# Performance work log

Hardware: AMD Instinct MI355X
Metric: run time of the kernel (lower is better)

The kernel has to match this reference:

```python
import jax, jax.numpy as jnp
import numpy as np

B, X, Y, Z, CIN = 4, 64, 64, 64, 32
COUT = 32
MX, MY, MZ = 16, 16, 16


def setup_inputs() -> dict:
    key = jax.random.key(0)
    k1, k2, k3 = jax.random.split(key, 3)
    x = jax.random.normal(k1, (B, X, Y, Z, CIN), dtype=jnp.float32)
    # Glorot-uniform-like scale for (in, out, mx, my, mz) weights
    fan = CIN + COUT
    lim = np.sqrt(6.0 / fan).astype(np.float32)
    w_real = jax.random.uniform(k2, (CIN, COUT, MX, MY, MZ), minval=-lim, maxval=lim, dtype=jnp.float32)
    w_imag = jax.random.uniform(k3, (CIN, COUT, MX, MY, MZ), minval=-lim, maxval=lim, dtype=jnp.float32)
    return {"x": x, "w_real": w_real, "w_imag": w_imag}


def reference(x, w_real, w_imag):
    # tf.signal.fft3d transforms the innermost 3 axes of the 5D input:
    # x is [B, X, Y, Z, C] so the FFT runs over (Y, Z, C) -- faithful to source.
    x_ft = jnp.fft.fftn(x.astype(jnp.complex64), axes=(-3, -2, -1))
    x_ft = jnp.transpose(x_ft, (0, 4, 1, 2, 3))            # [B, C, X, Y, Z]
    mx, my, mz = w_real.shape[2], w_real.shape[3], w_real.shape[4]
    x_crop = x_ft[:, :, :mx, :my, :mz]                     # [B, Cin, mx, my, mz]
    w = jax.lax.complex(w_real, w_imag)                    # [Cin, Cout, mx, my, mz]
    out_ft = jnp.einsum('bixyz,ioxyz->boxyz', x_crop, w)   # [B, Cout, mx, my, mz]
    sx, sy, sz = x.shape[1], x.shape[2], x.shape[3]
    out_ft = jnp.pad(out_ft, ((0, 0), (0, 0), (0, sx - mx), (0, sy - my), (0, sz - mz)))
    out_ft = jnp.transpose(out_ft, (0, 2, 3, 4, 1))        # [B, X, Y, Z, Cout]
    x_out = jnp.fft.ifftn(out_ft, axes=(-3, -2, -1))
    return jnp.real(x_out)
```

## Files before the change

kernel.cpp:

```cpp
#include <hip/hip_runtime.h>
#include <math.h>

#define PI_F 3.14159265358979323846f


__global__ __launch_bounds__(256) void k_dft_z(const float* __restrict__ x,
                                               float2* __restrict__ T1) {
    int bid = blockIdx.x;
    int ih = bid & 1, yg = (bid >> 1) & 7, xx = (bid >> 4) & 15, b = bid >> 8;
    __shared__ float  sx[8192];
    __shared__ float2 twt[1024];
    float4* sx4 = (float4*)sx;
    const float4* src4 = (const float4*)(x + (size_t)((b * 64 + xx) * 64 + yg * 8) * 2048) + ih * 4;
    #pragma unroll
    for (int t = threadIdx.x; t < 2048; t += 256) {
        int i4 = t & 3, z = (t >> 2) & 63, y = t >> 8;
        sx4[(y * 64 + z) * 4 + i4] = src4[(size_t)y * 512 + z * 8 + i4];
    }
    const float cn = -2.0f * PI_F / 64.0f;
    for (int t = threadIdx.x; t < 1024; t += 256) {
        int z = t >> 4, kz = t & 15;
        float a = cn * (float)((z * kz) & 63);
        twt[t] = make_float2(__cosf(a), __sinf(a));
    }
    __syncthreads();
    int ig = threadIdx.x & 3, kz2 = (threadIdx.x >> 2) & 7, y8 = threadIdx.x >> 5;
    float ar0[4], ai0[4], ar1[4], ai1[4];
    #pragma unroll
    for (int j = 0; j < 4; j++) { ar0[j] = ai0[j] = ar1[j] = ai1[j] = 0.f; }
    const float4* twv = (const float4*)twt;
    #pragma unroll 8
    for (int z = 0; z < 64; z++) {
        float4 va = sx4[(y8 * 64 + z) * 4 + ig];
        float4 tp = twv[z * 8 + kz2];
        float v[4] = {va.x, va.y, va.z, va.w};
        #pragma unroll
        for (int j = 0; j < 4; j++) {
            ar0[j] = fmaf(v[j], tp.x, ar0[j]);
            ai0[j] = fmaf(v[j], tp.y, ai0[j]);
            ar1[j] = fmaf(v[j], tp.z, ar1[j]);
            ai1[j] = fmaf(v[j], tp.w, ai1[j]);
        }
    }
    int y = yg * 8 + y8, kz0 = kz2 * 2, i0 = ih * 16 + ig * 4;
    float2* dst = T1 + (size_t)((b * 16 + xx) * 64 + y) * 512;
    float4* d0 = (float4*)(dst + kz0 * 32 + i0);
    d0[0] = make_float4(ar0[0], ai0[0], ar0[1], ai0[1]);
    d0[1] = make_float4(ar0[2], ai0[2], ar0[3], ai0[3]);
    float4* d1 = (float4*)(dst + (kz0 + 1) * 32 + i0);
    d1[0] = make_float4(ar1[0], ai1[0], ar1[1], ai1[1]);
    d1[1] = make_float4(ar1[2], ai1[2], ar1[3], ai1[3]);
}

__global__ __launch_bounds__(256) void k_dft_y(const float2* __restrict__ T1,
                                               float2* __restrict__ XH) {
    int bid = blockIdx.x;
    int ih = bid & 1, kzg = (bid >> 1) & 3, xx = (bid >> 3) & 15, b = bid >> 7;
    __shared__ float4 sT4[2304];
    __shared__ float2 twt[1024];
    const float4* Tg4 = (const float4*)T1;
    size_t gbase = (size_t)(b * 16 + xx) * 64 * 256;
    #pragma unroll
    for (int t = threadIdx.x; t < 2048; t += 256) {
        int i4 = t & 7, kz4 = (t >> 3) & 3, y = t >> 5;
        sT4[kz4 * 576 + y * 9 + i4] =
            Tg4[gbase + (size_t)y * 256 + (kzg * 4 + kz4) * 16 + ih * 8 + i4];
    }
    const float cn = -2.0f * PI_F / 64.0f;
    for (int t = threadIdx.x; t < 1024; t += 256) {
        int y = t >> 4, ky = t & 15;
        float a = cn * (float)((y * ky) & 63);
        twt[t] = make_float2(__cosf(a), __sinf(a));
    }
    __syncthreads();
    int ig = threadIdx.x & 7, ky2 = (threadIdx.x >> 3) & 7, kz4 = threadIdx.x >> 6;
    float ar[2][2], ai[2][2];
    #pragma unroll
    for (int h = 0; h < 2; h++) { ar[h][0] = ar[h][1] = ai[h][0] = ai[h][1] = 0.f; }
    const float4* twv = (const float4*)twt;
    #pragma unroll 8
    for (int y = 0; y < 64; y++) {
        float4 a  = sT4[kz4 * 576 + y * 9 + ig];
        float4 tp = twv[y * 8 + ky2];
        float xr[2] = {a.x, a.z}, xi[2] = {a.y, a.w};
        #pragma unroll
        for (int j = 0; j < 2; j++) {
            ar[0][j] += xr[j] * tp.x - xi[j] * tp.y;
            ai[0][j] += xr[j] * tp.y + xi[j] * tp.x;
            ar[1][j] += xr[j] * tp.z - xi[j] * tp.w;
            ai[1][j] += xr[j] * tp.w + xi[j] * tp.z;
        }
    }
    int kz = kzg * 4 + kz4;
    #pragma unroll
    for (int h = 0; h < 2; h++) {
        int ky = ky2 * 2 + h;
        float2* dp = XH + (((size_t)(b * 16 + xx) * 16 + ky) * 16 + kz) * 32 + ih * 16 + ig * 2;
        *(float4*)dp = make_float4(ar[h][0], ai[h][0], ar[h][1], ai[h][1]);
    }
}

__global__ __launch_bounds__(512) void k_mid(const float2* __restrict__ XH,
                                             const float* __restrict__ wr,
                                             const float* __restrict__ wi,
                                             float2* __restrict__ G,
                                             float* __restrict__ out) {
    int bid = blockIdx.x;
    if (bid >= 256) {
        int f = bid - 256;
        int b = f / 384, rem = f - b * 384;
        float4* d4 = (float4*)(out + (size_t)(b * 64 + 16) * 131072) + (size_t)rem * 4096;
        #pragma unroll
        for (int r = 0; r < 8; ++r)
            d4[r * 512 + threadIdx.x] = make_float4(0.f, 0.f, 0.f, 0.f);
        return;
    }
    int ky = bid & 15, xx = bid >> 4;
    __shared__ float2 sA[4 * 528];
    __shared__ float2 sB[4 * 576];
    __shared__ float2 twt[1024];
    for (int t = threadIdx.x; t < 2048; t += 512) {
        int b = t >> 9, kz = (t >> 5) & 15, i = t & 31;
        sA[b * 528 + kz * 33 + i] =
            XH[(((size_t)(b * 16 + xx) * 16 + ky) * 16 + kz) * 32 + i];
    }
    const float cn32 = -2.0f * PI_F / 32.0f;
    for (int t = threadIdx.x; t < 1024; t += 512) {
        int m = t >> 5, k = t & 31;
        float a = cn32 * (float)((m * k) & 31);
        twt[t] = make_float2(__cosf(a), __sinf(a));
    }
    __syncthreads();
    const float4* twv = (const float4*)twt;
    {
        int kz = threadIdx.x & 15, kig = (threadIdx.x >> 4) & 7, b = threadIdx.x >> 7;
        float xr[4], xi[4];
        #pragma unroll
        for (int j = 0; j < 4; j++) { xr[j] = xi[j] = 0.f; }
        #pragma unroll 8
        for (int i = 0; i < 32; i++) {
            float2 a   = sA[b * 528 + kz * 33 + i];
            float4 tp0 = twv[i * 16 + kig * 2];
            float4 tp1 = twv[i * 16 + kig * 2 + 1];
            xr[0] += a.x * tp0.x - a.y * tp0.y;  xi[0] += a.x * tp0.y + a.y * tp0.x;
            xr[1] += a.x * tp0.z - a.y * tp0.w;  xi[1] += a.x * tp0.w + a.y * tp0.z;
            xr[2] += a.x * tp1.x - a.y * tp1.y;  xi[2] += a.x * tp1.y + a.y * tp1.x;
            xr[3] += a.x * tp1.z - a.y * tp1.w;  xi[3] += a.x * tp1.w + a.y * tp1.z;
        }
        #pragma unroll
        for (int j = 0; j < 4; j++)
            sB[b * 576 + (kig * 4 + j) * 18 + kz] = make_float2(xr[j], xi[j]);
    }
    __syncthreads();
    {
        int kzg = threadIdx.x & 3, o = (threadIdx.x >> 2) & 31, b = threadIdx.x >> 7;
        int wbase = xx * 256 + ky * 16 + kzg * 4;
        float Fr[4], Fi[4];
        #pragma unroll
        for (int q = 0; q < 4; q++) { Fr[q] = Fi[q] = 0.f; }
        const float4* sB4 = (const float4*)sB;
        #pragma unroll 4
        for (int ki = 0; ki < 32; ki++) {
            float4 a01 = sB4[b * 288 + ki * 9 + kzg * 2];
            float4 a23 = sB4[b * 288 + ki * 9 + kzg * 2 + 1];
            float4 w4r = *(const float4*)(wr + (size_t)(ki * 32 + o) * 4096 + wbase);
            float4 w4i = *(const float4*)(wi + (size_t)(ki * 32 + o) * 4096 + wbase);
            float xr[4]  = {a01.x, a01.z, a23.x, a23.z};
            float xi[4]  = {a01.y, a01.w, a23.y, a23.w};
            float wrv[4] = {w4r.x, w4r.y, w4r.z, w4r.w};
            float wiv[4] = {w4i.x, w4i.y, w4i.z, w4i.w};
            #pragma unroll
            for (int q = 0; q < 4; q++) {
                Fr[q] += xr[q] * wrv[q] - xi[q] * wiv[q];
                Fi[q] += xr[q] * wiv[q] + xi[q] * wrv[q];
            }
        }
        #pragma unroll
        for (int q = 0; q < 4; q++) {
            int kz = kzg * 4 + q;
            sA[b * 528 + kz * 33 + o] = make_float2(Fr[q], Fi[q]);
        }
    }
    __syncthreads();
    {
        int kz = threadIdx.x & 15, cog = (threadIdx.x >> 4) & 7, b = threadIdx.x >> 7;
        float gr[4], gi[4];
        #pragma unroll
        for (int j = 0; j < 4; j++) { gr[j] = gi[j] = 0.f; }
        #pragma unroll 8
        for (int o = 0; o < 32; o++) {
            float2 f   = sA[b * 528 + kz * 33 + o];
            float4 tp0 = twv[o * 16 + cog * 2];
            float4 tp1 = twv[o * 16 + cog * 2 + 1];
            gr[0] += f.x * tp0.x + f.y * tp0.y;  gi[0] += f.y * tp0.x - f.x * tp0.y;
            gr[1] += f.x * tp0.z + f.y * tp0.w;  gi[1] += f.y * tp0.z - f.x * tp0.w;
            gr[2] += f.x * tp1.x + f.y * tp1.y;  gi[2] += f.y * tp1.x - f.x * tp1.y;
            gr[3] += f.x * tp1.z + f.y * tp1.w;  gi[3] += f.y * tp1.z - f.x * tp1.w;
        }
        float2* dp = G + (((size_t)(b * 16 + xx) * 16 + ky) * 16 + kz) * 32 + cog * 4;
        ((float4*)dp)[0] = make_float4(gr[0], gi[0], gr[1], gi[1]);
        ((float4*)dp)[1] = make_float4(gr[2], gi[2], gr[3], gi[3]);
    }
}

__global__ __launch_bounds__(256) void k_idft_zy(const float2* __restrict__ G,
                                                 float* __restrict__ out) {
    int bid = blockIdx.x;
    int ch = bid & 1, zc = (bid >> 1) & 7, xx = (bid >> 4) & 15, b = bid >> 8;
    float* dstb = out + (size_t)(b * 64 + xx) * 131072;
    __shared__ float2 sH[128 * 17];
    __shared__ float2 twy[1024];
    __shared__ float2 twz[8 * 17];
    const float cp = 2.0f * PI_F / 64.0f;
    for (int t = threadIdx.x; t < 1024; t += 256) {
        int ky = t >> 6, y = t & 63;
        float a = cp * (float)((ky * y) & 63);
        twy[t] = make_float2(__cosf(a), __sinf(a));
    }
    if (threadIdx.x < 128) {
        int dz = threadIdx.x >> 4, kz = threadIdx.x & 15;
        int z = zc * 8 + dz;
        float a = cp * (float)((kz * z) & 63);
        twz[dz * 17 + kz] = make_float2(__cosf(a), __sinf(a));
    }
    __syncthreads();
    {
        int co = threadIdx.x & 15, dz = (threadIdx.x >> 4) & 7, kyg = threadIdx.x >> 7;
        float tzc[16], tzs[16];
        #pragma unroll
        for (int kz = 0; kz < 16; ++kz) {
            float2 t = twz[dz * 17 + kz];
            tzc[kz] = t.x; tzs[kz] = t.y;
        }
        const float2* Gb0 = G + (size_t)(b * 16 + xx) * 16 * 512 + ch * 16 + co;
        #pragma unroll
        for (int t = 0; t < 8; ++t) {
            int ky = kyg * 8 + t;
            const float2* Gk = Gb0 + (size_t)ky * 512;
            float hr = 0.f, hi = 0.f;
            #pragma unroll
            for (int kz = 0; kz < 16; ++kz) {
                float2 g = Gk[kz * 32];
                hr += g.x * tzc[kz] - g.y * tzs[kz];
                hi += g.x * tzs[kz] + g.y * tzc[kz];
            }
            sH[(ky * 8 + dz) * 17 + co] = make_float2(hr, hi);
        }
    }
    __syncthreads();
    {
        int cog = threadIdx.x & 1, dz = (threadIdx.x >> 1) & 7, yg = threadIdx.x >> 4;
        float acc[4][8];
        #pragma unroll
        for (int yl = 0; yl < 4; yl++)
            #pragma unroll
            for (int cl = 0; cl < 8; cl++) acc[yl][cl] = 0.f;
        const float4* twy4 = (const float4*)twy;
        for (int ky = 0; ky < 16; ky++) {
            float4 t0 = twy4[ky * 32 + yg * 2 + 0];
            float4 t1 = twy4[ky * 32 + yg * 2 + 1];
            const float2* hp = sH + (ky * 8 + dz) * 17 + cog * 8;
            float hr[8], hi[8];
            #pragma unroll
            for (int cl = 0; cl < 8; ++cl) {
                float2 h = hp[cl];
                hr[cl] = h.x; hi[cl] = h.y;
            }
            float tc[4] = {t0.x, t0.z, t1.x, t1.z};
            float ts[4] = {t0.y, t0.w, t1.y, t1.w};
            #pragma unroll
            for (int yl = 0; yl < 4; yl++)
                #pragma unroll
                for (int cl = 0; cl < 8; cl++)
                    acc[yl][cl] += tc[yl] * hr[cl] - ts[yl] * hi[cl];
        }
        const float sc = 1.0f / 131072.0f;
        #pragma unroll
        for (int yl = 0; yl < 4; yl++) {
            int y = yg * 4 + yl;
            float4* d4 = (float4*)(dstb + ((size_t)y * 64 + zc * 8 + dz) * 32 + ch * 16 + cog * 8);
            d4[0] = make_float4(acc[yl][0] * sc, acc[yl][1] * sc, acc[yl][2] * sc, acc[yl][3] * sc);
            d4[1] = make_float4(acc[yl][4] * sc, acc[yl][5] * sc, acc[yl][6] * sc, acc[yl][7] * sc);
        }
    }
}

extern "C" void kernel_launch(void* const* d_in, const int* in_sizes, int n_in,
                              void* d_out, int out_size, void* d_ws, size_t ws_size,
                              hipStream_t stream) {
    const float* x  = (const float*)d_in[0];
    const float* wr = (const float*)d_in[1];
    const float* wi = (const float*)d_in[2];
    float* out = (float*)d_out;
    char*  ws  = (char*)d_ws;
    float2* T1 = (float2*)ws;
    float2* XH = (float2*)(ws + (size_t)16777216);
    float2* Gb = (float2*)(ws + (size_t)16777216 + 4194304);

    k_dft_z  <<<1024, 256, 0, stream>>>(x, T1);
    k_dft_y  <<< 512, 256, 0, stream>>>(T1, XH);
    k_mid    <<<1792, 512, 0, stream>>>(XH, wr, wi, Gb, out);
    k_idft_zy<<<1024, 256, 0, stream>>>(Gb, out);
}
```

Measured before the change: 312.7 us.

## Split inverse z/y DFT into two kernels with intermediate buffer

```diff
diff --git a/kernel.cpp b/kernel.cpp
--- a/kernel.cpp
+++ b/kernel.cpp
@@ -203,71 +203,84 @@
     }
 }
 
-__global__ __launch_bounds__(256) void k_idft_zy(const float2* __restrict__ G,
-                                                 float* __restrict__ out) {
-    int bid = blockIdx.x;
-    int ch = bid & 1, zc = (bid >> 1) & 7, xx = (bid >> 4) & 15, b = bid >> 8;
-    float* dstb = out + (size_t)(b * 64 + xx) * 131072;
-    __shared__ float2 sH[128 * 17];
-    __shared__ float2 twy[1024];
-    __shared__ float2 twz[8 * 17];
+__global__ __launch_bounds__(256) void k_idft_z(const float2* __restrict__ G,
+                                                float2* __restrict__ H) {
+    int bid = blockIdx.x;
+    int ky = bid & 15, xx = (bid >> 4) & 15, b = bid >> 8;
+    __shared__ float2 sG[512];
+    __shared__ float2 twz[1024];
+    size_t base = (((size_t)(b * 16 + xx) * 16 + ky)) * 512;
+    for (int t = threadIdx.x; t < 512; t += 256)
+        sG[t] = G[base + t];
     const float cp = 2.0f * PI_F / 64.0f;
     for (int t = threadIdx.x; t < 1024; t += 256) {
-        int ky = t >> 6, y = t & 63;
+        int z = t >> 4, kz = t & 15;
+        float a = cp * (float)((z * kz) & 63);
+        twz[t] = make_float2(__cosf(a), __sinf(a));
+    }
+    __syncthreads();
+    int co = threadIdx.x & 31, zq = threadIdx.x >> 5;
+    float2* Hb = H + (((size_t)(b * 16 + xx) * 16 + ky)) * 2048;
+    #pragma unroll
+    for (int j = 0; j < 8; ++j) {
+        int z = zq * 8 + j;
+        float r = 0.f, im = 0.f;
+        #pragma unroll
+        for (int kz = 0; kz < 16; ++kz) {
+            float2 t2 = twz[z * 16 + kz];
+            float2 g  = sG[kz * 32 + co];
+            r  += g.x * t2.x - g.y * t2.y;
+            im += g.x * t2.y + g.y * t2.x;
+        }
+        Hb[z * 32 + co] = make_float2(r, im);
+    }
+}
+
+__global__ __launch_bounds__(256) void k_idft_y(const float2* __restrict__ H,
+                                                float* __restrict__ out) {
+    int bid = blockIdx.x;
+    int yh = bid & 1, zc = (bid >> 1) & 7, xx = (bid >> 4) & 15, b = bid >> 8;
+    float* dstb = out + (size_t)(b * 64 + xx) * 131072;
+    __shared__ float2 sH[128 * 34];
+    __shared__ float2 twy[512];
+    {
+        const float2* Hb = H + ((size_t)(b * 16 + xx) * 16) * 2048 + (zc * 8) * 32;
+        float4* sH4w = (float4*)sH;
+        for (int t = threadIdx.x; t < 2048; t += 256) {
+            int row = t >> 4, idx = t & 15;
+            int ky = row >> 3, dz = row & 7;
+            float4 v = *(const float4*)(Hb + (size_t)ky * 2048 + dz * 32 + idx * 2);
+            sH4w[row * 17 + idx] = v;
+        }
+    }
+    const float cp = 2.0f * PI_F / 64.0f;
+    for (int t = threadIdx.x; t < 512; t += 256) {
+        int ky = t >> 5, yl = t & 31;
+        int y = yh * 32 + yl;
         float a = cp * (float)((ky * y) & 63);
-        twy[t] = make_float2(__cosf(a), __sinf(a));
-    }
-    if (threadIdx.x < 128) {
-        int dz = threadIdx.x >> 4, kz = threadIdx.x & 15;
-        int z = zc * 8 + dz;
-        float a = cp * (float)((kz * z) & 63);
-        twz[dz * 17 + kz] = make_float2(__cosf(a), __sinf(a));
-    }
-    __syncthreads();
-    {
-        int co = threadIdx.x & 15, dz = (threadIdx.x >> 4) & 7, kyg = threadIdx.x >> 7;
-        float tzc[16], tzs[16];
-        #pragma unroll
-        for (int kz = 0; kz < 16; ++kz) {
-            float2 t = twz[dz * 17 + kz];
-            tzc[kz] = t.x; tzs[kz] = t.y;
-        }
-        const float2* Gb0 = G + (size_t)(b * 16 + xx) * 16 * 512 + ch * 16 + co;
-        #pragma unroll
-        for (int t = 0; t < 8; ++t) {
-            int ky = kyg * 8 + t;
-            const float2* Gk = Gb0 + (size_t)ky * 512;
-            float hr = 0.f, hi = 0.f;
-            #pragma unroll
-            for (int kz = 0; kz < 16; ++kz) {
-                float2 g = Gk[kz * 32];
-                hr += g.x * tzc[kz] - g.y * tzs[kz];
-                hi += g.x * tzs[kz] + g.y * tzc[kz];
-            }
-            sH[(ky * 8 + dz) * 17 + co] = make_float2(hr, hi);
-        }
-    }
-    __syncthreads();
-    {
-        int cog = threadIdx.x & 1, dz = (threadIdx.x >> 1) & 7, yg = threadIdx.x >> 4;
+        twy[ky * 32 + yl] = make_float2(__cosf(a), __sinf(a));
+    }
+    __syncthreads();
+    {
+        int coq = threadIdx.x & 3, dz = (threadIdx.x >> 2) & 7, yg = threadIdx.x >> 5;
         float acc[4][8];
         #pragma unroll
         for (int yl = 0; yl < 4; yl++)
             #pragma unroll
             for (int cl = 0; cl < 8; cl++) acc[yl][cl] = 0.f;
         const float4* twy4 = (const float4*)twy;
+        const float4* sH4 = (const float4*)sH;
         for (int ky = 0; ky < 16; ky++) {
-            float4 t0 = twy4[ky * 32 + yg * 2 + 0];
-            float4 t1 = twy4[ky * 32 + yg * 2 + 1];
-            const float2* hp = sH + (ky * 8 + dz) * 17 + cog * 8;
-            float hr[8], hi[8];
-            #pragma unroll
-            for (int cl = 0; cl < 8; ++cl) {
-                float2 h = hp[cl];
-                hr[cl] = h.x; hi[cl] = h.y;
-            }
+            float4 t0 = twy4[ky * 16 + yg * 2 + 0];
+            float4 t1 = twy4[ky * 16 + yg * 2 + 1];
+            float4 h0 = sH4[(ky * 8 + dz) * 17 + coq * 4 + 0];
+            float4 h1 = sH4[(ky * 8 + dz) * 17 + coq * 4 + 1];
+            float4 h2 = sH4[(ky * 8 + dz) * 17 + coq * 4 + 2];
+            float4 h3 = sH4[(ky * 8 + dz) * 17 + coq * 4 + 3];
             float tc[4] = {t0.x, t0.z, t1.x, t1.z};
             float ts[4] = {t0.y, t0.w, t1.y, t1.w};
+            float hr[8] = {h0.x, h0.z, h1.x, h1.z, h2.x, h2.z, h3.x, h3.z};
+            float hi[8] = {h0.y, h0.w, h1.y, h1.w, h2.y, h2.w, h3.y, h3.w};
             #pragma unroll
             for (int yl = 0; yl < 4; yl++)
                 #pragma unroll
@@ -277,8 +290,8 @@
         const float sc = 1.0f / 131072.0f;
         #pragma unroll
         for (int yl = 0; yl < 4; yl++) {
-            int y = yg * 4 + yl;
-            float4* d4 = (float4*)(dstb + ((size_t)y * 64 + zc * 8 + dz) * 32 + ch * 16 + cog * 8);
+            int y = yh * 32 + yg * 4 + yl;
+            float4* d4 = (float4*)(dstb + ((size_t)y * 64 + zc * 8 + dz) * 32 + coq * 8);
             d4[0] = make_float4(acc[yl][0] * sc, acc[yl][1] * sc, acc[yl][2] * sc, acc[yl][3] * sc);
             d4[1] = make_float4(acc[yl][4] * sc, acc[yl][5] * sc, acc[yl][6] * sc, acc[yl][7] * sc);
         }
@@ -296,9 +309,11 @@
     float2* T1 = (float2*)ws;
     float2* XH = (float2*)(ws + (size_t)16777216);
     float2* Gb = (float2*)(ws + (size_t)16777216 + 4194304);
-
-    k_dft_z  <<<1024, 256, 0, stream>>>(x, T1);
-    k_dft_y  <<< 512, 256, 0, stream>>>(T1, XH);
-    k_mid    <<<1792, 512, 0, stream>>>(XH, wr, wi, Gb, out);
-    k_idft_zy<<<1024, 256, 0, stream>>>(Gb, out);
-}
+    float2* Hb = T1;
+
+    k_dft_z <<<1024, 256, 0, stream>>>(x, T1);
+    k_dft_y <<< 512, 256, 0, stream>>>(T1, XH);
+    k_mid   <<<1792, 512, 0, stream>>>(XH, wr, wi, Gb, out);
+    k_idft_z<<<1024, 256, 0, stream>>>(Gb, Hb);
+    k_idft_y<<<1024, 256, 0, stream>>>(Hb, out);
+}
```

Result: faster. 296.8 us (-5.1%).
